# Optimization experiments

Measured on AMD Instinct MI355X. Metric: run time of the kernel, lower is better.

The kernel has to match this reference:

```python
import jax, jax.numpy as jnp
import numpy as np

B, N, K, D = 8, 100000, 1024, 128  # batch, nodes, clusters, feature dim


def setup_inputs() -> dict:
    key = jax.random.key(0)
    k1, k2 = jax.random.split(key)
    x_batch = jax.random.normal(k1, (B, N, D), dtype=jnp.float32)
    # dense (K, N) weight as in the torch module, init U(-1/N, 1/N)
    weight = jax.random.uniform(k2, (K, N), dtype=jnp.float32,
                                minval=-1.0 / N, maxval=1.0 / N)
    # clustering: node i belongs to cluster i % K (a valid partition of N nodes)
    seg_ids = jnp.arange(N, dtype=jnp.int32) % K
    return {"x_batch": x_batch, "weight": weight, "seg_ids": seg_ids}


def reference(x_batch, weight, seg_ids):
    # Original: stack([(mask * weight) @ x for x in x_batch]) -> (B, K, D)
    # mask is one-hot per node (each node in exactly one cluster), so
    # (mask*weight) has a single nonzero per column: w_i = weight[seg_ids[i], i].
    # y[b, k] = sum_{i in C_k} w_i * x[b, i]  == segment-sum over nodes.
    n = x_batch.shape[1]
    k = weight.shape[0]
    w = weight[seg_ids, jnp.arange(n)]            # (N,) per-node weight
    wx = x_batch * w[None, :, None]               # (B, N, D)
    y = jax.ops.segment_sum(jnp.swapaxes(wx, 0, 1), seg_ids, num_segments=k)  # (K, B, D)
    return jnp.swapaxes(y, 0, 1)                  # (B, K, D)
```

## Files before the change

kernel.cpp:

```cpp
#include <hip/hip_runtime.h>


constexpr int D_CONST  = 128;
constexpr int D4_CONST = 32;
constexpr int MAX_CNT  = 128;

__global__ __launch_bounds__(256) void segpool_kernel(
    const float* __restrict__ x,
    const float* __restrict__ weight,
    const int*   __restrict__ seg,
    float*       __restrict__ out,
    int N, int K, int B, int npairs)
{
    __shared__ float s_w[4][MAX_CNT];

    const int wave = threadIdx.x >> 6;
    const int lane = threadIdx.x & 63;
    const int pair = blockIdx.x * 4 + wave;

    const bool active = (pair < npairs);
    int k = 0, b = 0, count = 0;
    if (active) {
        k = pair / B;
        b = pair - k * B;
        count = (N - 1 - k) / K + 1;
        for (int j = lane; j < count; j += 64) {
            const int i = k + j * K;
            s_w[wave][j] = weight[(size_t)seg[i] * N + i];
        }
    }
    __syncthreads();
    if (!active) return;

    const int d4   = lane & 31;
    const int half = lane >> 5;

    const float4* __restrict__ xb =
        reinterpret_cast<const float4*>(x) + (size_t)b * N * D4_CONST;

    float4 acc = make_float4(0.f, 0.f, 0.f, 0.f);

#pragma unroll 4
    for (int j = half; j < count; j += 2) {
        const float wv = s_w[wave][j];
        const float4 v = xb[(size_t)(k + j * K) * D4_CONST + d4];
        acc.x = fmaf(wv, v.x, acc.x);
        acc.y = fmaf(wv, v.y, acc.y);
        acc.z = fmaf(wv, v.z, acc.z);
        acc.w = fmaf(wv, v.w, acc.w);
    }

    acc.x += __shfl_down(acc.x, 32);
    acc.y += __shfl_down(acc.y, 32);
    acc.z += __shfl_down(acc.z, 32);
    acc.w += __shfl_down(acc.w, 32);

    if (half == 0) {
        float4* out4 = reinterpret_cast<float4*>(out);
        out4[((size_t)b * K + k) * D4_CONST + d4] = acc;
    }
}

extern "C" void kernel_launch(void* const* d_in, const int* in_sizes, int n_in,
                              void* d_out, int out_size, void* d_ws, size_t ws_size,
                              hipStream_t stream) {
    const float* x      = (const float*)d_in[0];
    const float* weight = (const float*)d_in[1];
    const int*   seg    = (const int*)  d_in[2];

    float* out = (float*)d_out;

    const int N = in_sizes[2];
    const int K = in_sizes[1] / N;
    const int B = in_sizes[0] / (N * D_CONST);

    const int npairs = B * K;
    const int grid   = (npairs + 3) / 4;

    segpool_kernel<<<grid, 256, 0, stream>>>(x, weight, seg, out, N, K, B, npairs);
}
```

Measured before the change: 690.0 us.

## Assign two adjacent clusters per wave for contiguous 1KB row reads

Each wave now handles two adjacent clusters (c0, c0+1) for one batch instead of one cluster split over two half-waves. Because adjacent nodes sit in adjacent clusters, each iteration reads 1KB of contiguous x rows across the full wave, and the final shuffle reduction goes away. The grid is reordered to be batch-major, and the weight gather is interleaved in shared memory. The code assumes K is divisible by 8 and relies on a guard for the uneven counts of the two clusters.

```diff
diff --git a/kernel.cpp b/kernel.cpp
--- a/kernel.cpp
+++ b/kernel.cpp
@@ -3,62 +3,61 @@
 
 constexpr int D_CONST  = 128;
 constexpr int D4_CONST = 32;
-constexpr int MAX_CNT  = 128;
+constexpr int JMAX     = 128;
 
-__global__ __launch_bounds__(256) void segpool_kernel(
+__global__ __launch_bounds__(256) void segpool_pair_kernel(
     const float* __restrict__ x,
     const float* __restrict__ weight,
     const int*   __restrict__ seg,
     float*       __restrict__ out,
-    int N, int K, int B, int npairs)
+    int N, int K, int B)
 {
-    __shared__ float s_w[4][MAX_CNT];
+    __shared__ float s_w[4][JMAX][2];
 
     const int wave = threadIdx.x >> 6;
     const int lane = threadIdx.x & 63;
-    const int pair = blockIdx.x * 4 + wave;
 
-    const bool active = (pair < npairs);
-    int k = 0, b = 0, count = 0;
-    if (active) {
-        k = pair / B;
-        b = pair - k * B;
-        count = (N - 1 - k) / K + 1;
-        for (int j = lane; j < count; j += 64) {
-            const int i = k + j * K;
-            s_w[wave][j] = weight[(size_t)seg[i] * N + i];
-        }
+    const int pairs_per_b  = K >> 1;
+    const int blocks_per_b = pairs_per_b >> 2;
+    const int b  = blockIdx.x / blocks_per_b;
+    const int p  = (blockIdx.x - b * blocks_per_b) * 4 + wave;
+    const int c0 = p << 1;
+    const int h  = lane >> 5;
+    const int c  = c0 + h;
+
+    const int cnt  = (N - 1 - c)  / K + 1;
+    const int cnt0 = (N - 1 - c0) / K + 1;
+
+    for (int idx = lane; idx < 2 * cnt0; idx += 64) {
+        const int j  = idx >> 1;
+        const int hh = idx & 1;
+        const int i  = j * K + c0 + hh;
+        float wv = 0.0f;
+        if (i < N) wv = weight[(size_t)seg[i] * N + i];
+        s_w[wave][j][hh] = wv;
     }
     __syncthreads();
-    if (!active) return;
 
-    const int d4   = lane & 31;
-    const int half = lane >> 5;
-
-    const float4* __restrict__ xb =
-        reinterpret_cast<const float4*>(x) + (size_t)b * N * D4_CONST;
+    const float4* __restrict__ x4 = reinterpret_cast<const float4*>(x);
+    const size_t base4   = ((size_t)b * N + c0) * D4_CONST + lane;
+    const size_t stride4 = (size_t)K * D4_CONST;
 
     float4 acc = make_float4(0.f, 0.f, 0.f, 0.f);
 
 #pragma unroll 4
-    for (int j = half; j < count; j += 2) {
-        const float wv = s_w[wave][j];
-        const float4 v = xb[(size_t)(k + j * K) * D4_CONST + d4];
-        acc.x = fmaf(wv, v.x, acc.x);
-        acc.y = fmaf(wv, v.y, acc.y);
-        acc.z = fmaf(wv, v.z, acc.z);
-        acc.w = fmaf(wv, v.w, acc.w);
+    for (int j = 0; j < cnt0; ++j) {
+        if (j < cnt) {
+            const float  wv = s_w[wave][j][h];
+            const float4 v  = x4[base4 + (size_t)j * stride4];
+            acc.x = fmaf(wv, v.x, acc.x);
+            acc.y = fmaf(wv, v.y, acc.y);
+            acc.z = fmaf(wv, v.z, acc.z);
+            acc.w = fmaf(wv, v.w, acc.w);
+        }
     }
 
-    acc.x += __shfl_down(acc.x, 32);
-    acc.y += __shfl_down(acc.y, 32);
-    acc.z += __shfl_down(acc.z, 32);
-    acc.w += __shfl_down(acc.w, 32);
-
-    if (half == 0) {
-        float4* out4 = reinterpret_cast<float4*>(out);
-        out4[((size_t)b * K + k) * D4_CONST + d4] = acc;
-    }
+    float4* __restrict__ out4 = reinterpret_cast<float4*>(out);
+    out4[((size_t)b * K + c0) * D4_CONST + lane] = acc;
 }
 
 extern "C" void kernel_launch(void* const* d_in, const int* in_sizes, int n_in,
@@ -74,8 +73,6 @@
     const int K = in_sizes[1] / N;
     const int B = in_sizes[0] / (N * D_CONST);
 
-    const int npairs = B * K;
-    const int grid   = (npairs + 3) / 4;
-
-    segpool_kernel<<<grid, 256, 0, stream>>>(x, weight, seg, out, N, K, B, npairs);
+    const int grid = B * (K / 8);
+    segpool_pair_kernel<<<grid, 256, 0, stream>>>(x, weight, seg, out, N, K, B);
 }
```

New measurement: 680.8 us. About the same (-1.3%).
